# Kernel optimization log

Measured on AMD Instinct MI355X. Metric: run time of the kernel, lower is better.

The kernel has to match this reference:

```python
import jax, jax.numpy as jnp
import numpy as np

DIM = 128          # per-stream channels (init arg `dim`)
C = 2 * DIM        # fused channels
NH = 8             # num_heads
HD = C // NH       # head_dim = 32
K = 3              # kernel_size
DIL = (2, 3)       # dilation list
ND = len(DIL)
SCALE = HD ** -0.5


def setup_inputs() -> dict:
    key = jax.random.key(0)
    ks = jax.random.split(key, 4)
    B, H, W = 4, 80, 80
    rgb = jax.random.normal(ks[0], (B, DIM, H, W), jnp.float32)
    ir = jax.random.normal(ks[1], (B, DIM, H, W), jnp.float32)
    w_qkv = jax.random.normal(ks[2], (3 * C, C), jnp.float32) * (C ** -0.5)
    w_proj = jax.random.normal(ks[3], (C, C), jnp.float32) * (C ** -0.5)
    b_proj = jnp.zeros((C,), jnp.float32)
    return {"rgb": rgb, "ir": ir, "w_qkv": w_qkv, "w_proj": w_proj, "b_proj": b_proj}


def _unfold(x, k, d):
    # nn.Unfold(k, dilation=d, padding=d*(k-1)//2, stride=1) -> [B, c, k*k, H, W]
    B, c, H, W = x.shape
    p = d * (k - 1) // 2
    xp = jnp.pad(x, ((0, 0), (0, 0), (p, p), (p, p)))
    pats = [xp[:, :, i * d:i * d + H, j * d:j * d + W]
            for i in range(k) for j in range(k)]
    return jnp.stack(pats, axis=2)


def _dilate_attention(q, k, v, d):
    # q,k,v: [B, c, H, W] with c = C // ND; attention over k*k dilated neighborhood
    B, c, H, W = q.shape
    h = c // HD
    N = H * W
    qr = q.reshape(B, h, HD, N)                      # [B,h,hd,N]
    ku = _unfold(k, K, d).reshape(B, h, HD, K * K, N)  # [B,h,hd,K2,N]
    vu = _unfold(v, K, d).reshape(B, h, HD, K * K, N)
    attn = jnp.einsum('bhdn,bhdkn->bhnk', qr, ku) * SCALE   # [B,h,N,K2]
    attn = jax.nn.softmax(attn, axis=-1)
    out = jnp.einsum('bhnk,bhdkn->bnhd', attn, vu)          # head-major channels
    return out.reshape(B, H, W, c)


def reference(rgb, ir, w_qkv, w_proj, b_proj):
    y = jnp.concatenate([rgb, ir], axis=1)            # [B, C, H, W]
    B, Cc, H, W = y.shape
    # 1x1 conv qkv, then split channels as [3, num_dilation, C//num_dilation]
    qkv = jnp.einsum('bchw,oc->bohw', y, w_qkv).reshape(B, 3, ND, Cc // ND, H, W)
    outs = [_dilate_attention(qkv[:, 0, i], qkv[:, 1, i], qkv[:, 2, i], DIL[i])
            for i in range(ND)]
    x = jnp.concatenate(outs, axis=-1)                # [B, H, W, C], dilation-major
    x = x @ w_proj.T + b_proj                         # proj Linear(C, C)
    # residual: add rgb to first half of channels, ir to second half
    return x + y.transpose(0, 2, 3, 1)
```

## Files before the change

### kernel.cpp

```cpp
#include <hip/hip_runtime.h>

#define HH 80
#define WW 80
#define NPIX 6400
#define NB 4
#define BN 25600
#define CDIM 256
#define QKVC 768
#define SCALE 0.17677669529663689f

typedef __attribute__((ext_vector_type(8))) short short8;
typedef __attribute__((ext_vector_type(4))) float floatx4;

__device__ __forceinline__ float b2f(ushort u) {
    return __uint_as_float(((uint)u) << 16);
}
__device__ __forceinline__ ushort f2b(float f) {
    uint u = __float_as_uint(f);
    return (ushort)((u + 0x7fffu + ((u >> 16) & 1u)) >> 16);
}
__device__ __forceinline__ void unpack8(uint4 v, float* f) {
    f[0] = __uint_as_float(v.x << 16); f[1] = __uint_as_float(v.x & 0xffff0000u);
    f[2] = __uint_as_float(v.y << 16); f[3] = __uint_as_float(v.y & 0xffff0000u);
    f[4] = __uint_as_float(v.z << 16); f[5] = __uint_as_float(v.z & 0xffff0000u);
    f[6] = __uint_as_float(v.w << 16); f[7] = __uint_as_float(v.w & 0xffff0000u);
}
__device__ __forceinline__ void gload_lds16(const void* gptr, void* lptr) {
    __builtin_amdgcn_global_load_lds(
        (const __attribute__((address_space(1))) unsigned int*)gptr,
        (__attribute__((address_space(3))) unsigned int*)lptr,
        16, 0, 0);
}

__global__ __launch_bounds__(256) void cast_w_k(
    const float* __restrict__ wq, const float* __restrict__ wp,
    ushort* __restrict__ wqb, ushort* __restrict__ wpb)
{
    int i = blockIdx.x * 256 + threadIdx.x;
    if (i < QKVC * CDIM) wqb[i] = f2b(wq[i]);
    if (i < CDIM * CDIM) wpb[i] = f2b(wp[i]);
}

__global__ __launch_bounds__(256) void cast_y_k(
    const float* __restrict__ rgb, const float* __restrict__ ir,
    ushort* __restrict__ Yb)
{
    __shared__ ushort T[32][72];
    const int tid = threadIdx.x;
    const int pix0 = blockIdx.x * 64;
    const int cb = blockIdx.y;
    const int b = blockIdx.z;

    const int pl = tid & 63, cg = tid >> 6;
    #pragma unroll
    for (int cc = 0; cc < 32; cc += 4) {
        int c = cb * 32 + cc + cg;
        const float* src = (c < 128) ? (rgb + ((size_t)b * 128 + c) * NPIX)
                                     : (ir + ((size_t)b * 128 + (c - 128)) * NPIX);
        T[cc + cg][pl] = f2b(src[pix0 + pl]);
    }
    __syncthreads();
    const int nl = tid >> 2, c0 = (tid & 3) * 8;
    ushort tmp[8];
    #pragma unroll
    for (int j = 0; j < 8; ++j) tmp[j] = T[c0 + j][nl];
    uint4 v;
    v.x = tmp[0] | ((uint)tmp[1] << 16);
    v.y = tmp[2] | ((uint)tmp[3] << 16);
    v.z = tmp[4] | ((uint)tmp[5] << 16);
    v.w = tmp[6] | ((uint)tmp[7] << 16);
    *(uint4*)(&Yb[((size_t)(b * NPIX + pix0 + nl)) * CDIM + cb * 32 + c0]) = v;
}

__device__ __forceinline__ void gemm_nt_body(
    const ushort* __restrict__ A, const ushort* __restrict__ W,
    ushort* As, ushort* Bs, int n0, int o0, floatx4 acc[4][4])
{
    const int tid = threadIdx.x;
    const int lane = tid & 63;
    const int wave = tid >> 6;
    const int wr = wave >> 1, wc = wave & 1;
    const int l15 = lane & 15, quad = lane >> 4;

    const int srow = tid >> 2;
    const int sk   = (tid & 3) * 8;

    for (int k0 = 0; k0 < CDIM; k0 += 32) {
        #pragma unroll
        for (int p = 0; p < 2; ++p) {
            gload_lds16(&A[(size_t)(n0 + p * 64 + srow) * CDIM + k0 + sk],
                        As + wave * 512 + p * 2048);
            gload_lds16(&W[(size_t)(o0 + p * 64 + srow) * CDIM + k0 + sk],
                        Bs + wave * 512 + p * 2048);
        }
        __syncthreads();
        short8 af[4], bfr[4];
        #pragma unroll
        for (int i = 0; i < 4; ++i)
            af[i] = *(const short8*)(&As[(wr * 64 + i * 16 + l15) * 32 + quad * 8]);
        #pragma unroll
        for (int j = 0; j < 4; ++j)
            bfr[j] = *(const short8*)(&Bs[(wc * 64 + j * 16 + l15) * 32 + quad * 8]);
        #pragma unroll
        for (int i = 0; i < 4; ++i)
            #pragma unroll
            for (int j = 0; j < 4; ++j)
                acc[i][j] = __builtin_amdgcn_mfma_f32_16x16x32_bf16(
                    af[i], bfr[j], acc[i][j], 0, 0, 0);
        __syncthreads();
    }
}

__global__ __launch_bounds__(256) void gemm_qkv_mfma(
    const ushort* __restrict__ Yb, const ushort* __restrict__ Wb,
    ushort* __restrict__ qkvb)
{
    __shared__ __align__(16) ushort As[128 * 32];
    __shared__ __align__(16) ushort Bs[128 * 32];
    const int tid = threadIdx.x;
    const int lane = tid & 63;
    const int wave = tid >> 6;
    const int wr = wave >> 1, wc = wave & 1;
    const int l15 = lane & 15, quad = lane >> 4;
    const int n0 = blockIdx.x * 128;
    const int o0 = blockIdx.y * 128;

    floatx4 acc[4][4] = {};
    gemm_nt_body(Yb, Wb, As, Bs, n0, o0, acc);

    #pragma unroll
    for (int i = 0; i < 4; ++i)
        #pragma unroll
        for (int j = 0; j < 4; ++j)
            #pragma unroll
            for (int r = 0; r < 4; ++r) {
                int n = n0 + wr * 64 + i * 16 + quad * 4 + r;
                int o = o0 + wc * 64 + j * 16 + l15;
                qkvb[(size_t)n * QKVC + o] = f2b(acc[i][j][r]);
            }
}

template<int D>
__device__ __forceinline__ void attn_tile(
    const ushort* __restrict__ qkvb, ushort* __restrict__ Xb,
    ushort* kl, int b, int dil_i, int head, int y0, int x0)
{
    constexpr int RW = 16 + 2 * D;
    constexpr int RP = RW * RW;
    const int tid = threadIdx.x;
    const int lane = tid & 63;
    const int wave = tid >> 6;
    const int obase = dil_i * 128 + head * 32;

    const int px = tid & 15, py = tid >> 4;
    const int n = b * NPIX + (y0 + py) * WW + (x0 + px);
    float q[32];
    {
        const uint4* qp = (const uint4*)(qkvb + (size_t)n * QKVC + obase);
        uint4 v0 = qp[0], v1 = qp[1], v2 = qp[2], v3 = qp[3];
        unpack8(v0, q); unpack8(v1, q + 8); unpack8(v2, q + 16); unpack8(v3, q + 24);
    }

    for (int p0 = 0; p0 < RP; p0 += 64) {
        int p = p0 + lane;
        int ry = p / RW, rx = p % RW;
        int gy = min(max(y0 - D + ry, 0), HH - 1);
        int gx = min(max(x0 - D + rx, 0), WW - 1);
        const ushort* row = qkvb + (size_t)(b * NPIX + gy * WW + gx) * QKVC + obase + wave * 8;
        if (p < RP)
            gload_lds16(row + 256, kl + (size_t)(wave * RP + p0) * 8);
    }
    __syncthreads();

    float sc[9];
    #pragma unroll
    for (int t = 0; t < 9; ++t) {
        const int dy = t / 3 - 1, dx = t % 3 - 1;
        const int yy = y0 + py + dy * D, xx = x0 + px + dx * D;
        const int p = (py + D + dy * D) * RW + (px + D + dx * D);
        float s = 0.f;
        if (yy >= 0 && yy < HH && xx >= 0 && xx < WW) {
            #pragma unroll
            for (int c = 0; c < 4; ++c) {
                float kv[8];
                unpack8(*(const uint4*)(kl + (size_t)(c * RP + p) * 8), kv);
                #pragma unroll
                for (int j = 0; j < 8; ++j) s += q[c * 8 + j] * kv[j];
            }
        }
        sc[t] = s * SCALE;
    }
    float m = sc[0];
    #pragma unroll
    for (int t = 1; t < 9; ++t) m = fmaxf(m, sc[t]);
    float sum = 0.f;
    #pragma unroll
    for (int t = 0; t < 9; ++t) { sc[t] = __expf(sc[t] - m); sum += sc[t]; }
    const float inv = 1.f / sum;

    __syncthreads();
    for (int p0 = 0; p0 < RP; p0 += 64) {
        int p = p0 + lane;
        int ry = p / RW, rx = p % RW;
        int gy = min(max(y0 - D + ry, 0), HH - 1);
        int gx = min(max(x0 - D + rx, 0), WW - 1);
        const ushort* row = qkvb + (size_t)(b * NPIX + gy * WW + gx) * QKVC + obase + wave * 8;
        if (p < RP)
            gload_lds16(row + 512, kl + (size_t)(wave * RP + p0) * 8);
    }
    __syncthreads();

    float o[32];
    #pragma unroll
    for (int hd = 0; hd < 32; ++hd) o[hd] = 0.f;
    #pragma unroll
    for (int t = 0; t < 9; ++t) {
        const int dy = t / 3 - 1, dx = t % 3 - 1;
        const int yy = y0 + py + dy * D, xx = x0 + px + dx * D;
        const int p = (py + D + dy * D) * RW + (px + D + dx * D);
        if (yy >= 0 && yy < HH && xx >= 0 && xx < WW) {
            const float wgt = sc[t] * inv;
            #pragma unroll
            for (int c = 0; c < 4; ++c) {
                float vv[8];
                unpack8(*(const uint4*)(kl + (size_t)(c * RP + p) * 8), vv);
                #pragma unroll
                for (int j = 0; j < 8; ++j) o[c * 8 + j] += wgt * vv[j];
            }
        }
    }
    uint4* xp = (uint4*)(Xb + (size_t)n * CDIM + obase);
    #pragma unroll
    for (int m4 = 0; m4 < 4; ++m4) {
        uint4 v;
        v.x = f2b(o[8 * m4 + 0]) | ((uint)f2b(o[8 * m4 + 1]) << 16);
        v.y = f2b(o[8 * m4 + 2]) | ((uint)f2b(o[8 * m4 + 3]) << 16);
        v.z = f2b(o[8 * m4 + 4]) | ((uint)f2b(o[8 * m4 + 5]) << 16);
        v.w = f2b(o[8 * m4 + 6]) | ((uint)f2b(o[8 * m4 + 7]) << 16);
        xp[m4] = v;
    }
}

__global__ __launch_bounds__(256) void attn2_k(
    const ushort* __restrict__ qkvb, ushort* __restrict__ Xb)
{
    __shared__ __align__(16) ushort kl[4 * 484 * 8];
    const int tile = blockIdx.x;
    const int y0 = (tile / 5) * 16, x0 = (tile % 5) * 16;
    const int dh = blockIdx.y;
    const int b = blockIdx.z;
    const int dil_i = dh >> 2, head = dh & 3;
    if (dil_i == 0) attn_tile<2>(qkvb, Xb, kl, b, 0, head, y0, x0);
    else            attn_tile<3>(qkvb, Xb, kl, b, 1, head, y0, x0);
}

__global__ __launch_bounds__(256) void proj_mfma(
    const ushort* __restrict__ Xb, const ushort* __restrict__ Wpb,
    const float* __restrict__ bp, const ushort* __restrict__ Yb,
    float* __restrict__ out)
{
    __shared__ __align__(16) ushort As[128 * 32];
    __shared__ __align__(16) ushort Bs[128 * 32];
    const int tid = threadIdx.x;
    const int lane = tid & 63;
    const int wave = tid >> 6;
    const int wr = wave >> 1, wc = wave & 1;
    const int l15 = lane & 15, quad = lane >> 4;
    const int n0 = blockIdx.x * 128;
    const int o0 = blockIdx.y * 128;

    floatx4 acc[4][4] = {};
    gemm_nt_body(Xb, Wpb, As, Bs, n0, o0, acc);

    #pragma unroll
    for (int i = 0; i < 4; ++i)
        #pragma unroll
        for (int j = 0; j < 4; ++j) {
            int o = o0 + wc * 64 + j * 16 + l15;
            float bias = bp[o];
            #pragma unroll
            for (int r = 0; r < 4; ++r) {
                int n = n0 + wr * 64 + i * 16 + quad * 4 + r;
                out[(size_t)n * CDIM + o] =
                    acc[i][j][r] + bias + b2f(Yb[(size_t)n * CDIM + o]);
            }
        }
}

extern "C" void kernel_launch(void* const* d_in, const int* in_sizes, int n_in,
                              void* d_out, int out_size, void* d_ws, size_t ws_size,
                              hipStream_t stream) {
    const float* rgb    = (const float*)d_in[0];
    const float* ir     = (const float*)d_in[1];
    const float* w_qkv  = (const float*)d_in[2];
    const float* w_proj = (const float*)d_in[3];
    const float* b_proj = (const float*)d_in[4];
    float* out = (float*)d_out;

    ushort* qkvb = (ushort*)d_ws;
    ushort* Yb   = qkvb + (size_t)BN * QKVC;
    ushort* Xb   = Yb + (size_t)BN * CDIM;
    ushort* Wqb  = Xb + (size_t)BN * CDIM;
    ushort* Wpb  = Wqb + (size_t)QKVC * CDIM;

    cast_w_k<<<QKVC, 256, 0, stream>>>(w_qkv, w_proj, Wqb, Wpb);
    cast_y_k<<<dim3(NPIX / 64, CDIM / 32, NB), 256, 0, stream>>>(rgb, ir, Yb);
    gemm_qkv_mfma<<<dim3(BN / 128, QKVC / 128), 256, 0, stream>>>(Yb, Wqb, qkvb);
    attn2_k<<<dim3(25, 8, NB), 256, 0, stream>>>(qkvb, Xb);
    proj_mfma<<<dim3(BN / 128, CDIM / 128), 256, 0, stream>>>(Xb, Wpb, b_proj, Yb, out);
}
```

Before: 149.9 us.

## Store qkv and attention output in head-chunked planar layout, fuse cast kernels

Changes the qkv workspace from pixel-major rows of 768 channels into 24 planes of 32 channels each, so each attention block gathers contiguous 64-byte rows per pixel for its head instead of strided slices of a 1.5KB row. The attention output is written in the same chunked layout, and the proj GEMM loads its A tiles from the matching plane for each k-chunk. The two cast kernels are also merged into one launch, with extra blocks handling the weight casts. The GEMM epilogue now writes 2-byte scattered stores with a 64-byte stride, which may cost more on the qkv write side.

```diff
diff --git a/kernel.cpp b/kernel.cpp
--- a/kernel.cpp
+++ b/kernel.cpp
@@ -32,21 +32,19 @@
         16, 0, 0);
 }
 
-__global__ __launch_bounds__(256) void cast_w_k(
+__global__ __launch_bounds__(256) void cast_all_k(
+    const float* __restrict__ rgb, const float* __restrict__ ir,
     const float* __restrict__ wq, const float* __restrict__ wp,
-    ushort* __restrict__ wqb, ushort* __restrict__ wpb)
-{
-    int i = blockIdx.x * 256 + threadIdx.x;
-    if (i < QKVC * CDIM) wqb[i] = f2b(wq[i]);
-    if (i < CDIM * CDIM) wpb[i] = f2b(wp[i]);
-}
-
-__global__ __launch_bounds__(256) void cast_y_k(
-    const float* __restrict__ rgb, const float* __restrict__ ir,
-    ushort* __restrict__ Yb)
-{
+    ushort* __restrict__ Yb, ushort* __restrict__ wqb, ushort* __restrict__ wpb)
+{
+    const int tid = threadIdx.x;
+    if (blockIdx.x >= 100) {
+        int i = (((blockIdx.x - 100) * 8 + blockIdx.y) * 4 + blockIdx.z) * 256 + tid;
+        if (i < QKVC * CDIM) wqb[i] = f2b(wq[i]);
+        else                 wpb[i - QKVC * CDIM] = f2b(wp[i - QKVC * CDIM]);
+        return;
+    }
     __shared__ ushort T[32][72];
-    const int tid = threadIdx.x;
     const int pix0 = blockIdx.x * 64;
     const int cb = blockIdx.y;
     const int b = blockIdx.z;
@@ -113,7 +111,7 @@
 
 __global__ __launch_bounds__(256) void gemm_qkv_mfma(
     const ushort* __restrict__ Yb, const ushort* __restrict__ Wb,
-    ushort* __restrict__ qkvb)
+    ushort* __restrict__ qkv2)
 {
     __shared__ __align__(16) ushort As[128 * 32];
     __shared__ __align__(16) ushort Bs[128 * 32];
@@ -131,32 +129,36 @@
     #pragma unroll
     for (int i = 0; i < 4; ++i)
         #pragma unroll
-        for (int j = 0; j < 4; ++j)
+        for (int j = 0; j < 4; ++j) {
+            const int o = o0 + wc * 64 + j * 16 + l15;
+            ushort* cbase = qkv2 + (size_t)(o >> 5) * BN * 32 + (o & 31);
             #pragma unroll
             for (int r = 0; r < 4; ++r) {
                 int n = n0 + wr * 64 + i * 16 + quad * 4 + r;
-                int o = o0 + wc * 64 + j * 16 + l15;
-                qkvb[(size_t)n * QKVC + o] = f2b(acc[i][j][r]);
+                cbase[(size_t)n * 32] = f2b(acc[i][j][r]);
             }
+        }
 }
 
 template<int D>
 __device__ __forceinline__ void attn_tile(
-    const ushort* __restrict__ qkvb, ushort* __restrict__ Xb,
-    ushort* kl, int b, int dil_i, int head, int y0, int x0)
+    const ushort* __restrict__ qkv2, ushort* __restrict__ X2,
+    ushort* kl, int b, int dh, int y0, int x0)
 {
     constexpr int RW = 16 + 2 * D;
     constexpr int RP = RW * RW;
     const int tid = threadIdx.x;
     const int lane = tid & 63;
     const int wave = tid >> 6;
-    const int obase = dil_i * 128 + head * 32;
+    const ushort* Qc = qkv2 + (size_t)dh * BN * 32;
+    const ushort* Kc = qkv2 + (size_t)(8 + dh) * BN * 32;
+    const ushort* Vc = qkv2 + (size_t)(16 + dh) * BN * 32;
 
     const int px = tid & 15, py = tid >> 4;
     const int n = b * NPIX + (y0 + py) * WW + (x0 + px);
     float q[32];
     {
-        const uint4* qp = (const uint4*)(qkvb + (size_t)n * QKVC + obase);
+        const uint4* qp = (const uint4*)(Qc + (size_t)n * 32);
         uint4 v0 = qp[0], v1 = qp[1], v2 = qp[2], v3 = qp[3];
         unpack8(v0, q); unpack8(v1, q + 8); unpack8(v2, q + 16); unpack8(v3, q + 24);
     }
@@ -166,9 +168,9 @@
         int ry = p / RW, rx = p % RW;
         int gy = min(max(y0 - D + ry, 0), HH - 1);
         int gx = min(max(x0 - D + rx, 0), WW - 1);
-        const ushort* row = qkvb + (size_t)(b * NPIX + gy * WW + gx) * QKVC + obase + wave * 8;
         if (p < RP)
-            gload_lds16(row + 256, kl + (size_t)(wave * RP + p0) * 8);
+            gload_lds16(Kc + (size_t)(b * NPIX + gy * WW + gx) * 32 + wave * 8,
+                        kl + (size_t)(wave * RP + p0) * 8);
     }
     __syncthreads();
 
@@ -204,9 +206,9 @@
         int ry = p / RW, rx = p % RW;
         int gy = min(max(y0 - D + ry, 0), HH - 1);
         int gx = min(max(x0 - D + rx, 0), WW - 1);
-        const ushort* row = qkvb + (size_t)(b * NPIX + gy * WW + gx) * QKVC + obase + wave * 8;
         if (p < RP)
-            gload_lds16(row + 512, kl + (size_t)(wave * RP + p0) * 8);
+            gload_lds16(Vc + (size_t)(b * NPIX + gy * WW + gx) * 32 + wave * 8,
+                        kl + (size_t)(wave * RP + p0) * 8);
     }
     __syncthreads();
 
@@ -229,7 +231,7 @@
             }
         }
     }
-    uint4* xp = (uint4*)(Xb + (size_t)n * CDIM + obase);
+    uint4* xp = (uint4*)(X2 + (size_t)dh * BN * 32 + (size_t)n * 32);
     #pragma unroll
     for (int m4 = 0; m4 < 4; ++m4) {
         uint4 v;
@@ -242,20 +244,19 @@
 }
 
 __global__ __launch_bounds__(256) void attn2_k(
-    const ushort* __restrict__ qkvb, ushort* __restrict__ Xb)
+    const ushort* __restrict__ qkv2, ushort* __restrict__ X2)
 {
     __shared__ __align__(16) ushort kl[4 * 484 * 8];
     const int tile = blockIdx.x;
     const int y0 = (tile / 5) * 16, x0 = (tile % 5) * 16;
     const int dh = blockIdx.y;
     const int b = blockIdx.z;
-    const int dil_i = dh >> 2, head = dh & 3;
-    if (dil_i == 0) attn_tile<2>(qkvb, Xb, kl, b, 0, head, y0, x0);
-    else            attn_tile<3>(qkvb, Xb, kl, b, 1, head, y0, x0);
+    if (dh < 4) attn_tile<2>(qkv2, X2, kl, b, dh, y0, x0);
+    else        attn_tile<3>(qkv2, X2, kl, b, dh, y0, x0);
 }
 
 __global__ __launch_bounds__(256) void proj_mfma(
-    const ushort* __restrict__ Xb, const ushort* __restrict__ Wpb,
+    const ushort* __restrict__ X2, const ushort* __restrict__ Wpb,
     const float* __restrict__ bp, const ushort* __restrict__ Yb,
     float* __restrict__ out)
 {
@@ -269,8 +270,36 @@
     const int n0 = blockIdx.x * 128;
     const int o0 = blockIdx.y * 128;
 
+    const int srow = tid >> 2;
+    const int sk   = (tid & 3) * 8;
+
     floatx4 acc[4][4] = {};
-    gemm_nt_body(Xb, Wpb, As, Bs, n0, o0, acc);
+
+    for (int k0 = 0; k0 < CDIM; k0 += 32) {
+        const ushort* Achunk = X2 + (size_t)(k0 >> 5) * BN * 32;
+        #pragma unroll
+        for (int p = 0; p < 2; ++p) {
+            gload_lds16(&Achunk[(size_t)(n0 + p * 64 + srow) * 32 + sk],
+                        As + wave * 512 + p * 2048);
+            gload_lds16(&Wpb[(size_t)(o0 + p * 64 + srow) * CDIM + k0 + sk],
+                        Bs + wave * 512 + p * 2048);
+        }
+        __syncthreads();
+        short8 af[4], bfr[4];
+        #pragma unroll
+        for (int i = 0; i < 4; ++i)
+            af[i] = *(const short8*)(&As[(wr * 64 + i * 16 + l15) * 32 + quad * 8]);
+        #pragma unroll
+        for (int j = 0; j < 4; ++j)
+            bfr[j] = *(const short8*)(&Bs[(wc * 64 + j * 16 + l15) * 32 + quad * 8]);
+        #pragma unroll
+        for (int i = 0; i < 4; ++i)
+            #pragma unroll
+            for (int j = 0; j < 4; ++j)
+                acc[i][j] = __builtin_amdgcn_mfma_f32_16x16x32_bf16(
+                    af[i], bfr[j], acc[i][j], 0, 0, 0);
+        __syncthreads();
+    }
 
     #pragma unroll
     for (int i = 0; i < 4; ++i)
@@ -297,15 +326,15 @@
     const float* b_proj = (const float*)d_in[4];
     float* out = (float*)d_out;
 
-    ushort* qkvb = (ushort*)d_ws;
-    ushort* Yb   = qkvb + (size_t)BN * QKVC;
-    ushort* Xb   = Yb + (size_t)BN * CDIM;
-    ushort* Wqb  = Xb + (size_t)BN * CDIM;
+    ushort* qkv2 = (ushort*)d_ws;
+    ushort* Yb   = qkv2 + (size_t)24 * BN * 32;
+    ushort* X2   = Yb + (size_t)BN * CDIM;
+    ushort* Wqb  = X2 + (size_t)8 * BN * 32;
     ushort* Wpb  = Wqb + (size_t)QKVC * CDIM;
 
-    cast_w_k<<<QKVC, 256, 0, stream>>>(w_qkv, w_proj, Wqb, Wpb);
-    cast_y_k<<<dim3(NPIX / 64, CDIM / 32, NB), 256, 0, stream>>>(rgb, ir, Yb);
-    gemm_qkv_mfma<<<dim3(BN / 128, QKVC / 128), 256, 0, stream>>>(Yb, Wqb, qkvb);
-    attn2_k<<<dim3(25, 8, NB), 256, 0, stream>>>(qkvb, Xb);
-    proj_mfma<<<dim3(BN / 128, CDIM / 128), 256, 0, stream>>>(Xb, Wpb, b_proj, Yb, out);
-}
+    cast_all_k<<<dim3(132, 8, NB), 256, 0, stream>>>(rgb, ir, w_qkv, w_proj,
+                                                     Yb, Wqb, Wpb);
+    gemm_qkv_mfma<<<dim3(BN / 128, QKVC / 128), 256, 0, stream>>>(Yb, Wqb, qkv2);
+    attn2_k<<<dim3(25, 8, NB), 256, 0, stream>>>(qkv2, X2);
+    proj_mfma<<<dim3(BN / 128, CDIM / 128), 256, 0, stream>>>(X2, Wpb, b_proj, Yb, out);
+}
```

Result: faster. 140.0 us (-6.6%).
